# Kernel tuning notes

Hardware: AMD Instinct MI355X
Metric: run time of the kernel (lower is better)

Reference implementation:

```python
import jax, jax.numpy as jnp
import numpy as np

N = 50000      # num nodes
HID = 64       # hidden_dim
N2V = 64       # node2vec dim
E = 800000     # num edges
EP = 100000    # prediction edges
L = 2          # num_layers
EPS = 1e-5     # BatchNorm eps


def setup_inputs() -> dict:
    key = jax.random.key(0)
    ks = jax.random.split(key, 8)
    edge_index = jax.random.randint(ks[0], (2, E), 0, N)
    pred_edge = jax.random.randint(ks[1], (EP, 2), 0, N)
    id_emb = jax.random.normal(ks[2], (N, HID), jnp.float32) * 0.1      # learnable ID embedding
    n2v_emb = jax.random.normal(ks[3], (N, N2V), jnp.float32) * 0.1     # frozen node2vec embedding
    proj_w = jax.random.normal(ks[4], (HID + N2V, HID), jnp.float32) / np.sqrt(HID + N2V)
    proj_b = jnp.zeros((HID,), jnp.float32)
    conv_w = jax.random.normal(ks[5], (L, HID, HID), jnp.float32) / np.sqrt(HID)
    conv_b = jnp.zeros((L, HID), jnp.float32)
    bn_gamma = jnp.ones((L, HID), jnp.float32)
    bn_beta = jnp.zeros((L, HID), jnp.float32)
    return {"edge_index": edge_index, "pred_edge": pred_edge, "id_emb": id_emb,
            "n2v_emb": n2v_emb, "proj_w": proj_w, "proj_b": proj_b,
            "conv_w": conv_w, "conv_b": conv_b, "bn_gamma": bn_gamma, "bn_beta": bn_beta}


def reference(edge_index, pred_edge, id_emb, n2v_emb, proj_w, proj_b, conv_w, conv_b, bn_gamma, bn_beta):
    # input projection of concatenated embeddings: [N, HID+N2V] @ [HID+N2V, HID]
    x = jnp.concatenate([id_emb, n2v_emb], axis=1) @ proj_w + proj_b

    # GCN normalization with self-loops: norm_e = d^-1/2[src] * d^-1/2[dst]
    loops = jnp.arange(N, dtype=edge_index.dtype)
    row = jnp.concatenate([edge_index[0], loops])   # source nodes
    col = jnp.concatenate([edge_index[1], loops])   # destination nodes
    deg = jax.ops.segment_sum(jnp.ones(row.shape, x.dtype), col, num_segments=N)
    dis = jnp.where(deg > 0, jax.lax.rsqrt(deg), 0.0)
    norm = dis[row] * dis[col]                      # [E+N]

    for l in range(L):
        h = x @ conv_w[l]                                                    # [N, HID]
        agg = jax.ops.segment_sum(norm[:, None] * h[row], col, num_segments=N) + conv_b[l]
        # BatchNorm1d (training-mode batch stats over nodes)
        mu = agg.mean(axis=0)
        var = agg.var(axis=0)
        xn = (agg - mu) * jax.lax.rsqrt(var + EPS) * bn_gamma[l] + bn_beta[l]
        x = x + jax.nn.relu(xn)                                              # residual (shapes match)

    # dot-product link decoder
    z = x
    return (z[pred_edge[:, 0]] * z[pred_edge[:, 1]]).sum(axis=1)
```

## Files before the change

### kernel.cpp

```cpp
#include <hip/hip_runtime.h>

#define NN 50000
#define HID 64
#define NE 800000
#define NP 100000
#define BN_EPS 1e-5f
#define NB1 196

static inline size_t alignup(size_t x) { return (x + 255) & ~(size_t)255; }

__device__ __forceinline__ void f4fma(float a, const float4& w, float4& c) {
    c.x += a * w.x; c.y += a * w.y; c.z += a * w.z; c.w += a * w.w;
}
__device__ __forceinline__ void f4acc(float w, const float4& a, float4& c) {
    c.x += w * a.x; c.y += w * a.y; c.z += w * a.z; c.w += w * a.w;
}
__device__ __forceinline__ unsigned bfpack(float a, float b) {
    unsigned ua = __float_as_uint(a), ub = __float_as_uint(b);
    ua = (ua + 0x7fffu + ((ua >> 16) & 1u)) >> 16;
    ub = (ub + 0x7fffu + ((ub >> 16) & 1u)) >> 16;
    return ua | (ub << 16);
}
__device__ __forceinline__ float4 bf2f4(uint2 u) {
    float4 r;
    r.x = __uint_as_float(u.x << 16);
    r.y = __uint_as_float(u.x & 0xffff0000u);
    r.z = __uint_as_float(u.y << 16);
    r.w = __uint_as_float(u.y & 0xffff0000u);
    return r;
}


__global__ __launch_bounds__(256) void k_zero(int* __restrict__ cnt, float* __restrict__ sums) {
    int i = blockIdx.x * blockDim.x + threadIdx.x;
    if (i < NN) cnt[i] = 0;
    if (i < 256) sums[i] = 0.f;
}


__global__ __launch_bounds__(256) void k_count(const int* __restrict__ col,
                                               int* __restrict__ cnt, int* __restrict__ rank) {
    int e = blockIdx.x * blockDim.x + threadIdx.x;
    if (e < NE) rank[e] = atomicAdd(&cnt[col[e]], 1);
}


__global__ __launch_bounds__(256) void k_scan1(const int* __restrict__ cnt,
                                               int* __restrict__ offs, int* __restrict__ bsum,
                                               float* __restrict__ dis) {
    __shared__ int s[256];
    int t = threadIdx.x;
    int i = blockIdx.x * 256 + t;
    int v = (i < NN) ? cnt[i] : 0;
    if (i < NN) dis[i] = rsqrtf((float)(v + 1));
    s[t] = v;
    __syncthreads();
    for (int off = 1; off < 256; off <<= 1) {
        int add = (t >= off) ? s[t - off] : 0;
        __syncthreads();
        s[t] += add;
        __syncthreads();
    }
    if (i < NN) offs[i] = s[t] - v;
    if (t == 255) bsum[blockIdx.x] = s[255];
}

__global__ __launch_bounds__(256) void k_scan2(int* __restrict__ bsum, int* __restrict__ boff) {
    __shared__ int s[256];
    int t = threadIdx.x;
    int v = (t < NB1) ? bsum[t] : 0;
    s[t] = v;
    __syncthreads();
    for (int off = 1; off < 256; off <<= 1) {
        int add = (t >= off) ? s[t - off] : 0;
        __syncthreads();
        s[t] += add;
        __syncthreads();
    }
    if (t < NB1) boff[t] = s[t] - v;
}

__global__ __launch_bounds__(256) void k_scan3(int* __restrict__ offs, const int* __restrict__ boff) {
    int i = blockIdx.x * blockDim.x + threadIdx.x;
    if (i < NN) offs[i] += boff[i >> 8];
    if (i == 0) offs[NN] = NE;
}


__global__ __launch_bounds__(256) void k_fill(const int* __restrict__ row, const int* __restrict__ col,
                                              const int* __restrict__ rank, const int* __restrict__ offs,
                                              const float* __restrict__ dis,
                                              int2* __restrict__ csr) {
    int e = blockIdx.x * blockDim.x + threadIdx.x;
    if (e >= NE) return;
    int s = row[e], d = col[e];
    int2 v;
    v.x = s;
    v.y = __float_as_int(dis[s] * dis[d]);
    csr[offs[d] + rank[e]] = v;
}


__global__ __launch_bounds__(256) void k_proj(const float* __restrict__ id_emb,
                                              const float* __restrict__ n2v,
                                              const float* __restrict__ W,
                                              const float* __restrict__ b,
                                              float* __restrict__ x,
                                              unsigned short* __restrict__ xh) {
    __shared__ float Wl[128 * 64];
    int tid = threadIdx.x;
    for (int i = tid; i < 128 * 64; i += 256) Wl[i] = W[i];
    __syncthreads();
    int sub = tid >> 4, q = tid & 15;
    const float4* W4 = (const float4*)Wl;
    const float4* id4 = (const float4*)id_emb;
    const float4* nv4 = (const float4*)n2v;
    float4* x4 = (float4*)x;
    uint2* xh2 = (uint2*)xh;
    float4 bb = ((const float4*)b)[q];
    const int ngroups = (NN + 63) / 64;
    for (int g = blockIdx.x; g < ngroups; g += gridDim.x) {
        int n0 = g * 64 + sub * 4;
        int r0 = min(n0 + 0, NN - 1), r1 = min(n0 + 1, NN - 1);
        int r2 = min(n0 + 2, NN - 1), r3 = min(n0 + 3, NN - 1);
        float4 c0 = bb, c1 = bb, c2 = bb, c3 = bb;
#pragma unroll 4
        for (int k4 = 0; k4 < 16; ++k4) {
            float4 a0 = id4[r0 * 16 + k4];
            float4 a1 = id4[r1 * 16 + k4];
            float4 a2 = id4[r2 * 16 + k4];
            float4 a3 = id4[r3 * 16 + k4];
            float4 w0 = W4[(k4 * 4 + 0) * 16 + q];
            float4 w1 = W4[(k4 * 4 + 1) * 16 + q];
            float4 w2 = W4[(k4 * 4 + 2) * 16 + q];
            float4 w3 = W4[(k4 * 4 + 3) * 16 + q];
            f4fma(a0.x, w0, c0); f4fma(a0.y, w1, c0); f4fma(a0.z, w2, c0); f4fma(a0.w, w3, c0);
            f4fma(a1.x, w0, c1); f4fma(a1.y, w1, c1); f4fma(a1.z, w2, c1); f4fma(a1.w, w3, c1);
            f4fma(a2.x, w0, c2); f4fma(a2.y, w1, c2); f4fma(a2.z, w2, c2); f4fma(a2.w, w3, c2);
            f4fma(a3.x, w0, c3); f4fma(a3.y, w1, c3); f4fma(a3.z, w2, c3); f4fma(a3.w, w3, c3);
        }
#pragma unroll 4
        for (int k4 = 0; k4 < 16; ++k4) {
            float4 a0 = nv4[r0 * 16 + k4];
            float4 a1 = nv4[r1 * 16 + k4];
            float4 a2 = nv4[r2 * 16 + k4];
            float4 a3 = nv4[r3 * 16 + k4];
            float4 w0 = W4[(k4 * 4 + 64) * 16 + q];
            float4 w1 = W4[(k4 * 4 + 65) * 16 + q];
            float4 w2 = W4[(k4 * 4 + 66) * 16 + q];
            float4 w3 = W4[(k4 * 4 + 67) * 16 + q];
            f4fma(a0.x, w0, c0); f4fma(a0.y, w1, c0); f4fma(a0.z, w2, c0); f4fma(a0.w, w3, c0);
            f4fma(a1.x, w0, c1); f4fma(a1.y, w1, c1); f4fma(a1.z, w2, c1); f4fma(a1.w, w3, c1);
            f4fma(a2.x, w0, c2); f4fma(a2.y, w1, c2); f4fma(a2.z, w2, c2); f4fma(a2.w, w3, c2);
            f4fma(a3.x, w0, c3); f4fma(a3.y, w1, c3); f4fma(a3.z, w2, c3); f4fma(a3.w, w3, c3);
        }
        if (n0 + 0 < NN) { x4[(n0+0)*16+q] = c0; xh2[(n0+0)*16+q] = make_uint2(bfpack(c0.x,c0.y), bfpack(c0.z,c0.w)); }
        if (n0 + 1 < NN) { x4[(n0+1)*16+q] = c1; xh2[(n0+1)*16+q] = make_uint2(bfpack(c1.x,c1.y), bfpack(c1.z,c1.w)); }
        if (n0 + 2 < NN) { x4[(n0+2)*16+q] = c2; xh2[(n0+2)*16+q] = make_uint2(bfpack(c2.x,c2.y), bfpack(c2.z,c2.w)); }
        if (n0 + 3 < NN) { x4[(n0+3)*16+q] = c3; xh2[(n0+3)*16+q] = make_uint2(bfpack(c3.x,c3.y), bfpack(c3.z,c3.w)); }
    }
}


__global__ __launch_bounds__(256) void k_gather(const int* __restrict__ offs,
                                                const int2* __restrict__ csr,
                                                const float* __restrict__ dis,
                                                const float* __restrict__ x,
                                                const unsigned short* __restrict__ xh,
                                                unsigned short* __restrict__ th) {
    int gw = (blockIdx.x * blockDim.x + threadIdx.x) >> 6;
    int lane = threadIdx.x & 63;
    int sub = lane >> 4, q = lane & 15;
    int node = gw * 4 + sub;
    if (node >= NN) return;
    const float4* x4 = (const float4*)x;
    const uint2* xh2 = (const uint2*)xh;
    float di = dis[node];
    float dd = di * di;
    float4 v = x4[node * 16 + q];
    float4 acc = make_float4(dd * v.x, dd * v.y, dd * v.z, dd * v.w);
    int j = offs[node], j1 = offs[node + 1];
    for (; j + 7 < j1; j += 8) {
        int2 e0 = csr[j],     e1 = csr[j + 1], e2 = csr[j + 2], e3 = csr[j + 3];
        int2 e4 = csr[j + 4], e5 = csr[j + 5], e6 = csr[j + 6], e7 = csr[j + 7];
        uint2 u0 = xh2[e0.x * 16 + q];
        uint2 u1 = xh2[e1.x * 16 + q];
        uint2 u2 = xh2[e2.x * 16 + q];
        uint2 u3 = xh2[e3.x * 16 + q];
        uint2 u4 = xh2[e4.x * 16 + q];
        uint2 u5 = xh2[e5.x * 16 + q];
        uint2 u6 = xh2[e6.x * 16 + q];
        uint2 u7 = xh2[e7.x * 16 + q];
        f4acc(__int_as_float(e0.y), bf2f4(u0), acc);
        f4acc(__int_as_float(e1.y), bf2f4(u1), acc);
        f4acc(__int_as_float(e2.y), bf2f4(u2), acc);
        f4acc(__int_as_float(e3.y), bf2f4(u3), acc);
        f4acc(__int_as_float(e4.y), bf2f4(u4), acc);
        f4acc(__int_as_float(e5.y), bf2f4(u5), acc);
        f4acc(__int_as_float(e6.y), bf2f4(u6), acc);
        f4acc(__int_as_float(e7.y), bf2f4(u7), acc);
    }
    for (; j < j1; ++j) {
        int2 e0 = csr[j];
        uint2 u0 = xh2[e0.x * 16 + q];
        f4acc(__int_as_float(e0.y), bf2f4(u0), acc);
    }
    ((uint2*)th)[node * 16 + q] = make_uint2(bfpack(acc.x, acc.y), bfpack(acc.z, acc.w));
}


__global__ __launch_bounds__(256) void k_gemm_stats(const unsigned short* __restrict__ th,
                                                    const float* __restrict__ W,
                                                    float* __restrict__ agg,
                                                    float* __restrict__ sums) {
    __shared__ float Wl[64 * 64];
    __shared__ float ls0[16][64];
    __shared__ float ls1[16][64];
    int tid = threadIdx.x;
    for (int i = tid; i < 64 * 64; i += 256) Wl[i] = W[i];
    __syncthreads();
    int sub = tid >> 4, q = tid & 15;
    const uint2* t2 = (const uint2*)th;
    const float4* W4 = (const float4*)Wl;
    float4* agg4 = (float4*)agg;
    float4 s1 = make_float4(0.f, 0.f, 0.f, 0.f), s2 = s1;
    const int ngroups = (NN + 63) / 64;
    for (int g = blockIdx.x; g < ngroups; g += gridDim.x) {
        int n0 = g * 64 + sub * 4;
        int r0 = min(n0 + 0, NN - 1), r1 = min(n0 + 1, NN - 1);
        int r2 = min(n0 + 2, NN - 1), r3 = min(n0 + 3, NN - 1);
        float4 c0 = make_float4(0.f,0.f,0.f,0.f), c1 = c0, c2 = c0, c3 = c0;
#pragma unroll 4
        for (int k4 = 0; k4 < 16; ++k4) {
            float4 a0 = bf2f4(t2[r0 * 16 + k4]);
            float4 a1 = bf2f4(t2[r1 * 16 + k4]);
            float4 a2 = bf2f4(t2[r2 * 16 + k4]);
            float4 a3 = bf2f4(t2[r3 * 16 + k4]);
            float4 w0 = W4[(k4 * 4 + 0) * 16 + q];
            float4 w1 = W4[(k4 * 4 + 1) * 16 + q];
            float4 w2 = W4[(k4 * 4 + 2) * 16 + q];
            float4 w3 = W4[(k4 * 4 + 3) * 16 + q];
            f4fma(a0.x, w0, c0); f4fma(a0.y, w1, c0); f4fma(a0.z, w2, c0); f4fma(a0.w, w3, c0);
            f4fma(a1.x, w0, c1); f4fma(a1.y, w1, c1); f4fma(a1.z, w2, c1); f4fma(a1.w, w3, c1);
            f4fma(a2.x, w0, c2); f4fma(a2.y, w1, c2); f4fma(a2.z, w2, c2); f4fma(a2.w, w3, c2);
            f4fma(a3.x, w0, c3); f4fma(a3.y, w1, c3); f4fma(a3.z, w2, c3); f4fma(a3.w, w3, c3);
        }
        if (n0 + 0 < NN) { agg4[(n0 + 0) * 16 + q] = c0;
            s1.x += c0.x; s1.y += c0.y; s1.z += c0.z; s1.w += c0.w;
            s2.x += c0.x*c0.x; s2.y += c0.y*c0.y; s2.z += c0.z*c0.z; s2.w += c0.w*c0.w; }
        if (n0 + 1 < NN) { agg4[(n0 + 1) * 16 + q] = c1;
            s1.x += c1.x; s1.y += c1.y; s1.z += c1.z; s1.w += c1.w;
            s2.x += c1.x*c1.x; s2.y += c1.y*c1.y; s2.z += c1.z*c1.z; s2.w += c1.w*c1.w; }
        if (n0 + 2 < NN) { agg4[(n0 + 2) * 16 + q] = c2;
            s1.x += c2.x; s1.y += c2.y; s1.z += c2.z; s1.w += c2.w;
            s2.x += c2.x*c2.x; s2.y += c2.y*c2.y; s2.z += c2.z*c2.z; s2.w += c2.w*c2.w; }
        if (n0 + 3 < NN) { agg4[(n0 + 3) * 16 + q] = c3;
            s1.x += c3.x; s1.y += c3.y; s1.z += c3.z; s1.w += c3.w;
            s2.x += c3.x*c3.x; s2.y += c3.y*c3.y; s2.z += c3.z*c3.z; s2.w += c3.w*c3.w; }
    }
    ls0[sub][q * 4 + 0] = s1.x; ls0[sub][q * 4 + 1] = s1.y;
    ls0[sub][q * 4 + 2] = s1.z; ls0[sub][q * 4 + 3] = s1.w;
    ls1[sub][q * 4 + 0] = s2.x; ls1[sub][q * 4 + 1] = s2.y;
    ls1[sub][q * 4 + 2] = s2.z; ls1[sub][q * 4 + 3] = s2.w;
    __syncthreads();
    if (tid < 64) {
        float a = 0.f;
#pragma unroll
        for (int r = 0; r < 16; ++r) a += ls0[r][tid];
        atomicAdd(&sums[tid], a);
    } else if (tid < 128) {
        int c = tid - 64;
        float a = 0.f;
#pragma unroll
        for (int r = 0; r < 16; ++r) a += ls1[r][c];
        atomicAdd(&sums[64 + c], a);
    }
}


__global__ __launch_bounds__(256) void k_bnupdate(const float* __restrict__ agg,
                                                  const float* __restrict__ sums,
                                                  const float* __restrict__ gamma,
                                                  const float* __restrict__ beta,
                                                  float* __restrict__ x,
                                                  unsigned short* __restrict__ xh) {
    int i = blockIdx.x * blockDim.x + threadIdx.x;
    if (i >= NN * 16) return;
    int f4 = i & 15;
    const float invn = 1.0f / (float)NN;
    float4 sm = ((const float4*)sums)[f4];
    float4 sq = ((const float4*)(sums + 64))[f4];
    float4 g = ((const float4*)gamma)[f4];
    float4 be = ((const float4*)beta)[f4];
    float4 a = ((const float4*)agg)[i];
    float4 xv = ((const float4*)x)[i];
    float mu, var, rstd, xn;
    mu = sm.x * invn; var = sq.x * invn - mu * mu; rstd = rsqrtf(var + BN_EPS);
    xn = (a.x - mu) * rstd * g.x + be.x; xv.x += fmaxf(xn, 0.f);
    mu = sm.y * invn; var = sq.y * invn - mu * mu; rstd = rsqrtf(var + BN_EPS);
    xn = (a.y - mu) * rstd * g.y + be.y; xv.y += fmaxf(xn, 0.f);
    mu = sm.z * invn; var = sq.z * invn - mu * mu; rstd = rsqrtf(var + BN_EPS);
    xn = (a.z - mu) * rstd * g.z + be.z; xv.z += fmaxf(xn, 0.f);
    mu = sm.w * invn; var = sq.w * invn - mu * mu; rstd = rsqrtf(var + BN_EPS);
    xn = (a.w - mu) * rstd * g.w + be.w; xv.w += fmaxf(xn, 0.f);
    ((float4*)x)[i] = xv;
    ((uint2*)xh)[i] = make_uint2(bfpack(xv.x, xv.y), bfpack(xv.z, xv.w));
}


__global__ __launch_bounds__(256) void k_decode(const int* __restrict__ pred,
                                                const unsigned short* __restrict__ zh,
                                                float* __restrict__ out) {
    int gw = (blockIdx.x * blockDim.x + threadIdx.x) >> 6;
    int lane = threadIdx.x & 63;
    int sub = lane >> 4, q = lane & 15;
    int p = gw * 4 + sub;
    if (p >= NP) return;
    const uint2* z2 = (const uint2*)zh;
    int a = pred[2 * p], b = pred[2 * p + 1];
    float4 va = bf2f4(z2[a * 16 + q]);
    float4 vb = bf2f4(z2[b * 16 + q]);
    float v = va.x * vb.x + va.y * vb.y + va.z * vb.z + va.w * vb.w;
    v += __shfl_xor(v, 1);
    v += __shfl_xor(v, 2);
    v += __shfl_xor(v, 4);
    v += __shfl_xor(v, 8);
    if (q == 0) out[p] = v;
}

extern "C" void kernel_launch(void* const* d_in, const int* in_sizes, int n_in,
                              void* d_out, int out_size, void* d_ws, size_t ws_size,
                              hipStream_t stream) {
    const int* edge_index = (const int*)d_in[0];
    const int* pred       = (const int*)d_in[1];
    const float* id_emb   = (const float*)d_in[2];
    const float* n2v      = (const float*)d_in[3];
    const float* proj_w   = (const float*)d_in[4];
    const float* proj_b   = (const float*)d_in[5];
    const float* conv_w   = (const float*)d_in[6];
    const float* gamma    = (const float*)d_in[8];
    const float* beta     = (const float*)d_in[9];
    float* out = (float*)d_out;

    char* ws = (char*)d_ws;
    size_t off = 0;
    float* dis  = (float*)(ws + off); off += alignup(NN * 4);
    int* cnt    = (int*)(ws + off);   off += alignup(NN * 4);
    int* offs   = (int*)(ws + off);   off += alignup((NN + 1) * 4);
    int* rank   = (int*)(ws + off);   off += alignup((size_t)NE * 4);
    int* bsum   = (int*)(ws + off);   off += alignup(NB1 * 4);
    int* boff   = (int*)(ws + off);   off += alignup(NB1 * 4);
    int2* csr   = (int2*)(ws + off);  off += alignup((size_t)NE * 8);
    float* x    = (float*)(ws + off); off += alignup((size_t)NN * 64 * 4);
    float* agg  = (float*)(ws + off); off += alignup((size_t)NN * 64 * 4);
    unsigned short* xh = (unsigned short*)(ws + off); off += alignup((size_t)NN * 64 * 2);
    unsigned short* th = (unsigned short*)(ws + off); off += alignup((size_t)NN * 64 * 2);
    float* sums = (float*)(ws + off);

    const int* row = edge_index;
    const int* col = edge_index + NE;

    k_zero<<<NB1, 256, 0, stream>>>(cnt, sums);
    k_count<<<(NE + 255) / 256, 256, 0, stream>>>(col, cnt, rank);
    k_scan1<<<NB1, 256, 0, stream>>>(cnt, offs, bsum, dis);
    k_scan2<<<1, 256, 0, stream>>>(bsum, boff);
    k_scan3<<<NB1, 256, 0, stream>>>(offs, boff);
    k_fill<<<(NE + 255) / 256, 256, 0, stream>>>(row, col, rank, offs, dis, csr);

    k_proj<<<512, 256, 0, stream>>>(id_emb, n2v, proj_w, proj_b, x, xh);

    for (int l = 0; l < 2; ++l) {
        k_gather<<<((NN + 3) / 4 * 64 + 255) / 256, 256, 0, stream>>>(offs, csr, dis, x, xh, th);
        k_gemm_stats<<<512, 256, 0, stream>>>(th, conv_w + l * 64 * 64, agg, sums + l * 128);
        k_bnupdate<<<(NN * 16 + 255) / 256, 256, 0, stream>>>(agg, sums + l * 128, gamma + l * 64, beta + l * 64, x, xh);
    }

    k_decode<<<(NP / 4 * 64 + 255) / 256, 256, 0, stream>>>(pred, xh, out);
}
```

Before: 213.0 us.

## Factor GCN edge norm into per-node prescale, drop per-edge weights from CSR

The symmetric normalisation dis[src]*dis[dst] is split into two per-node factors. Source features are stored in bf16 already multiplied by dis[src] (in the projection kernel and in the layer-0 BN update), and the gather multiplies the plain neighbour sum by dis[dst] at the end. The CSR shrinks from int2 (source plus weight) to int (source only), halving the edge-list traffic in the gather and fill kernels and removing the per-edge dis lookups in fill. In exchange, the prescale rounds dis*x to bf16 rather than x alone, and the last layer writes unscaled xh so the decoder still sees z.

New measurement: 207.6 us. 2.6% less time.

```diff
diff --git a/kernel.cpp b/kernel.cpp
--- a/kernel.cpp
+++ b/kernel.cpp
@@ -12,8 +12,8 @@
 __device__ __forceinline__ void f4fma(float a, const float4& w, float4& c) {
     c.x += a * w.x; c.y += a * w.y; c.z += a * w.z; c.w += a * w.w;
 }
-__device__ __forceinline__ void f4acc(float w, const float4& a, float4& c) {
-    c.x += w * a.x; c.y += w * a.y; c.z += w * a.z; c.w += w * a.w;
+__device__ __forceinline__ void f4add(const float4& a, float4& c) {
+    c.x += a.x; c.y += a.y; c.z += a.z; c.w += a.w;
 }
 __device__ __forceinline__ unsigned bfpack(float a, float b) {
     unsigned ua = __float_as_uint(a), ub = __float_as_uint(b);
@@ -89,15 +89,10 @@
 
 __global__ __launch_bounds__(256) void k_fill(const int* __restrict__ row, const int* __restrict__ col,
                                               const int* __restrict__ rank, const int* __restrict__ offs,
-                                              const float* __restrict__ dis,
-                                              int2* __restrict__ csr) {
+                                              int* __restrict__ csr_src) {
     int e = blockIdx.x * blockDim.x + threadIdx.x;
     if (e >= NE) return;
-    int s = row[e], d = col[e];
-    int2 v;
-    v.x = s;
-    v.y = __float_as_int(dis[s] * dis[d]);
-    csr[offs[d] + rank[e]] = v;
+    csr_src[offs[col[e]] + rank[e]] = row[e];
 }
 
 
@@ -105,6 +100,7 @@
                                               const float* __restrict__ n2v,
                                               const float* __restrict__ W,
                                               const float* __restrict__ b,
+                                              const float* __restrict__ dis,
                                               float* __restrict__ x,
                                               unsigned short* __restrict__ xh) {
     __shared__ float Wl[128 * 64];
@@ -154,16 +150,20 @@
             f4fma(a2.x, w0, c2); f4fma(a2.y, w1, c2); f4fma(a2.z, w2, c2); f4fma(a2.w, w3, c2);
             f4fma(a3.x, w0, c3); f4fma(a3.y, w1, c3); f4fma(a3.z, w2, c3); f4fma(a3.w, w3, c3);
         }
-        if (n0 + 0 < NN) { x4[(n0+0)*16+q] = c0; xh2[(n0+0)*16+q] = make_uint2(bfpack(c0.x,c0.y), bfpack(c0.z,c0.w)); }
-        if (n0 + 1 < NN) { x4[(n0+1)*16+q] = c1; xh2[(n0+1)*16+q] = make_uint2(bfpack(c1.x,c1.y), bfpack(c1.z,c1.w)); }
-        if (n0 + 2 < NN) { x4[(n0+2)*16+q] = c2; xh2[(n0+2)*16+q] = make_uint2(bfpack(c2.x,c2.y), bfpack(c2.z,c2.w)); }
-        if (n0 + 3 < NN) { x4[(n0+3)*16+q] = c3; xh2[(n0+3)*16+q] = make_uint2(bfpack(c3.x,c3.y), bfpack(c3.z,c3.w)); }
+        if (n0 + 0 < NN) { float d = dis[n0+0]; x4[(n0+0)*16+q] = c0;
+            xh2[(n0+0)*16+q] = make_uint2(bfpack(c0.x*d,c0.y*d), bfpack(c0.z*d,c0.w*d)); }
+        if (n0 + 1 < NN) { float d = dis[n0+1]; x4[(n0+1)*16+q] = c1;
+            xh2[(n0+1)*16+q] = make_uint2(bfpack(c1.x*d,c1.y*d), bfpack(c1.z*d,c1.w*d)); }
+        if (n0 + 2 < NN) { float d = dis[n0+2]; x4[(n0+2)*16+q] = c2;
+            xh2[(n0+2)*16+q] = make_uint2(bfpack(c2.x*d,c2.y*d), bfpack(c2.z*d,c2.w*d)); }
+        if (n0 + 3 < NN) { float d = dis[n0+3]; x4[(n0+3)*16+q] = c3;
+            xh2[(n0+3)*16+q] = make_uint2(bfpack(c3.x*d,c3.y*d), bfpack(c3.z*d,c3.w*d)); }
     }
 }
 
 
 __global__ __launch_bounds__(256) void k_gather(const int* __restrict__ offs,
-                                                const int2* __restrict__ csr,
+                                                const int* __restrict__ csr_src,
                                                 const float* __restrict__ dis,
                                                 const float* __restrict__ x,
                                                 const unsigned short* __restrict__ xh,
@@ -175,36 +175,34 @@
     if (node >= NN) return;
     const float4* x4 = (const float4*)x;
     const uint2* xh2 = (const uint2*)xh;
-    float di = dis[node];
-    float dd = di * di;
-    float4 v = x4[node * 16 + q];
-    float4 acc = make_float4(dd * v.x, dd * v.y, dd * v.z, dd * v.w);
+    float4 acc = make_float4(0.f, 0.f, 0.f, 0.f);
     int j = offs[node], j1 = offs[node + 1];
     for (; j + 7 < j1; j += 8) {
-        int2 e0 = csr[j],     e1 = csr[j + 1], e2 = csr[j + 2], e3 = csr[j + 3];
-        int2 e4 = csr[j + 4], e5 = csr[j + 5], e6 = csr[j + 6], e7 = csr[j + 7];
-        uint2 u0 = xh2[e0.x * 16 + q];
-        uint2 u1 = xh2[e1.x * 16 + q];
-        uint2 u2 = xh2[e2.x * 16 + q];
-        uint2 u3 = xh2[e3.x * 16 + q];
-        uint2 u4 = xh2[e4.x * 16 + q];
-        uint2 u5 = xh2[e5.x * 16 + q];
-        uint2 u6 = xh2[e6.x * 16 + q];
-        uint2 u7 = xh2[e7.x * 16 + q];
-        f4acc(__int_as_float(e0.y), bf2f4(u0), acc);
-        f4acc(__int_as_float(e1.y), bf2f4(u1), acc);
-        f4acc(__int_as_float(e2.y), bf2f4(u2), acc);
-        f4acc(__int_as_float(e3.y), bf2f4(u3), acc);
-        f4acc(__int_as_float(e4.y), bf2f4(u4), acc);
-        f4acc(__int_as_float(e5.y), bf2f4(u5), acc);
-        f4acc(__int_as_float(e6.y), bf2f4(u6), acc);
-        f4acc(__int_as_float(e7.y), bf2f4(u7), acc);
+        int s0 = csr_src[j],     s1 = csr_src[j + 1], s2 = csr_src[j + 2], s3 = csr_src[j + 3];
+        int s4 = csr_src[j + 4], s5 = csr_src[j + 5], s6 = csr_src[j + 6], s7 = csr_src[j + 7];
+        uint2 u0 = xh2[s0 * 16 + q];
+        uint2 u1 = xh2[s1 * 16 + q];
+        uint2 u2 = xh2[s2 * 16 + q];
+        uint2 u3 = xh2[s3 * 16 + q];
+        uint2 u4 = xh2[s4 * 16 + q];
+        uint2 u5 = xh2[s5 * 16 + q];
+        uint2 u6 = xh2[s6 * 16 + q];
+        uint2 u7 = xh2[s7 * 16 + q];
+        f4add(bf2f4(u0), acc); f4add(bf2f4(u1), acc);
+        f4add(bf2f4(u2), acc); f4add(bf2f4(u3), acc);
+        f4add(bf2f4(u4), acc); f4add(bf2f4(u5), acc);
+        f4add(bf2f4(u6), acc); f4add(bf2f4(u7), acc);
     }
     for (; j < j1; ++j) {
-        int2 e0 = csr[j];
-        uint2 u0 = xh2[e0.x * 16 + q];
-        f4acc(__int_as_float(e0.y), bf2f4(u0), acc);
-    }
+        uint2 u0 = xh2[csr_src[j] * 16 + q];
+        f4add(bf2f4(u0), acc);
+    }
+    float di = dis[node];
+    float4 v = x4[node * 16 + q];
+    acc.x = di * (acc.x + di * v.x);
+    acc.y = di * (acc.y + di * v.y);
+    acc.z = di * (acc.z + di * v.z);
+    acc.w = di * (acc.w + di * v.w);
     ((uint2*)th)[node * 16 + q] = make_uint2(bfpack(acc.x, acc.y), bfpack(acc.z, acc.w));
 }
 
@@ -282,6 +280,8 @@
                                                   const float* __restrict__ sums,
                                                   const float* __restrict__ gamma,
                                                   const float* __restrict__ beta,
+                                                  const float* __restrict__ dis,
+                                                  int prescale,
                                                   float* __restrict__ x,
                                                   unsigned short* __restrict__ xh) {
     int i = blockIdx.x * blockDim.x + threadIdx.x;
@@ -304,7 +304,8 @@
     mu = sm.w * invn; var = sq.w * invn - mu * mu; rstd = rsqrtf(var + BN_EPS);
     xn = (a.w - mu) * rstd * g.w + be.w; xv.w += fmaxf(xn, 0.f);
     ((float4*)x)[i] = xv;
-    ((uint2*)xh)[i] = make_uint2(bfpack(xv.x, xv.y), bfpack(xv.z, xv.w));
+    float d = prescale ? dis[i >> 4] : 1.0f;
+    ((uint2*)xh)[i] = make_uint2(bfpack(xv.x * d, xv.y * d), bfpack(xv.z * d, xv.w * d));
 }
 
 
@@ -344,18 +345,18 @@
 
     char* ws = (char*)d_ws;
     size_t off = 0;
-    float* dis  = (float*)(ws + off); off += alignup(NN * 4);
-    int* cnt    = (int*)(ws + off);   off += alignup(NN * 4);
-    int* offs   = (int*)(ws + off);   off += alignup((NN + 1) * 4);
-    int* rank   = (int*)(ws + off);   off += alignup((size_t)NE * 4);
-    int* bsum   = (int*)(ws + off);   off += alignup(NB1 * 4);
-    int* boff   = (int*)(ws + off);   off += alignup(NB1 * 4);
-    int2* csr   = (int2*)(ws + off);  off += alignup((size_t)NE * 8);
-    float* x    = (float*)(ws + off); off += alignup((size_t)NN * 64 * 4);
-    float* agg  = (float*)(ws + off); off += alignup((size_t)NN * 64 * 4);
+    float* dis   = (float*)(ws + off); off += alignup(NN * 4);
+    int* cnt     = (int*)(ws + off);   off += alignup(NN * 4);
+    int* offs    = (int*)(ws + off);   off += alignup((NN + 1) * 4);
+    int* rank    = (int*)(ws + off);   off += alignup((size_t)NE * 4);
+    int* bsum    = (int*)(ws + off);   off += alignup(NB1 * 4);
+    int* boff    = (int*)(ws + off);   off += alignup(NB1 * 4);
+    int* csr_src = (int*)(ws + off);   off += alignup((size_t)NE * 4);
+    float* x     = (float*)(ws + off); off += alignup((size_t)NN * 64 * 4);
+    float* agg   = (float*)(ws + off); off += alignup((size_t)NN * 64 * 4);
     unsigned short* xh = (unsigned short*)(ws + off); off += alignup((size_t)NN * 64 * 2);
     unsigned short* th = (unsigned short*)(ws + off); off += alignup((size_t)NN * 64 * 2);
-    float* sums = (float*)(ws + off);
+    float* sums  = (float*)(ws + off);
 
     const int* row = edge_index;
     const int* col = edge_index + NE;
@@ -365,14 +366,15 @@
     k_scan1<<<NB1, 256, 0, stream>>>(cnt, offs, bsum, dis);
     k_scan2<<<1, 256, 0, stream>>>(bsum, boff);
     k_scan3<<<NB1, 256, 0, stream>>>(offs, boff);
-    k_fill<<<(NE + 255) / 256, 256, 0, stream>>>(row, col, rank, offs, dis, csr);
-
-    k_proj<<<512, 256, 0, stream>>>(id_emb, n2v, proj_w, proj_b, x, xh);
+    k_fill<<<(NE + 255) / 256, 256, 0, stream>>>(row, col, rank, offs, csr_src);
+
+    k_proj<<<512, 256, 0, stream>>>(id_emb, n2v, proj_w, proj_b, dis, x, xh);
 
     for (int l = 0; l < 2; ++l) {
-        k_gather<<<((NN + 3) / 4 * 64 + 255) / 256, 256, 0, stream>>>(offs, csr, dis, x, xh, th);
+        k_gather<<<((NN + 3) / 4 * 64 + 255) / 256, 256, 0, stream>>>(offs, csr_src, dis, x, xh, th);
         k_gemm_stats<<<512, 256, 0, stream>>>(th, conv_w + l * 64 * 64, agg, sums + l * 128);
-        k_bnupdate<<<(NN * 16 + 255) / 256, 256, 0, stream>>>(agg, sums + l * 128, gamma + l * 64, beta + l * 64, x, xh);
+        k_bnupdate<<<(NN * 16 + 255) / 256, 256, 0, stream>>>(agg, sums + l * 128, gamma + l * 64,
+                                                              beta + l * 64, dis, (l == 0) ? 1 : 0, x, xh);
     }
 
     k_decode<<<(NP / 4 * 64 + 255) / 256, 256, 0, stream>>>(pred, xh, out);
```
